# Optimization experiments

Measured on AMD Instinct MI355X. Metric: run time of the kernel, lower is better.

## Reference

```python
import jax, jax.numpy as jnp
import numpy as np

B, S, D, H = 2, 2048, 1024, 16
DH = D // H  # 64
NEG = -1000000000.0


def setup_inputs() -> dict:
    key = jax.random.key(0)
    ks = jax.random.split(key, 10)
    scale = 1.0 / np.sqrt(D)
    inp = {
        "x": jax.random.normal(ks[0], (B, S, D), dtype=jnp.float32),
        "mask": jax.random.randint(ks[1], (B, S, S), 0, 2, dtype=jnp.int32),
        "Wq": jax.random.normal(ks[2], (D, D), dtype=jnp.float32) * scale,
        "bq": jnp.zeros((D,), dtype=jnp.float32),
        "Wk": jax.random.normal(ks[3], (D, D), dtype=jnp.float32) * scale,
        "bk": jnp.zeros((D,), dtype=jnp.float32),
        "Wv": jax.random.normal(ks[4], (D, D), dtype=jnp.float32) * scale,
        "bv": jnp.zeros((D,), dtype=jnp.float32),
        "Wo": jax.random.normal(ks[5], (D, D), dtype=jnp.float32) * scale,
        "bo": jnp.zeros((D,), dtype=jnp.float32),
    }
    return inp


def reference(x, mask, Wq, bq, Wk, bk, Wv, bv, Wo, bo):
    b, s, _ = x.shape
    # Linear projections (torch Linear: y = x @ W^T + b), then split heads -> [b,h,s,dh]
    q = (x @ Wq.T + bq).reshape(b, s, H, DH).transpose(0, 2, 1, 3)
    k = (x @ Wk.T + bk).reshape(b, s, H, DH).transpose(0, 2, 1, 3)
    v = (x @ Wv.T + bv).reshape(b, s, H, DH).transpose(0, 2, 1, 3)
    # scores: [b,h,sq,sk]
    scores = jnp.einsum("bhqd,bhkd->bhqk", q, k) / jnp.sqrt(jnp.float32(DH))
    # code masks where mask == 0 (mask broadcast over heads)
    scores = jnp.where(mask[:, None, :, :] == 0, NEG, scores)
    attn = jax.nn.softmax(scores, axis=-1)
    out = jnp.einsum("bhqk,bhkd->bhqd", attn, v)  # [b,h,sq,dh]
    out = out.transpose(0, 2, 1, 3).reshape(b, s, D)  # merge heads -> [b,s,d]
    return out @ Wo.T + bo
```

## Files before the change

### kernel.cpp

```cpp
#include <hip/hip_runtime.h>
#include <stdint.h>

#define SB 2
#define SS 2048
#define SD 1024
#define SH 16
#define SDH 64
#define SM (SB*SS)
#define NEGINF_MASK -1000000000.0f
#define QSCALE 0.18033688011112043f
#define CSHIFT 16.0f

typedef __attribute__((ext_vector_type(8))) short short8;
typedef __attribute__((ext_vector_type(4))) short short4v;
typedef __attribute__((ext_vector_type(4))) float f32x4;
typedef __attribute__((ext_vector_type(4))) float float4v;
typedef __attribute__((ext_vector_type(4))) uint32_t uint4v;

__device__ static inline short f2bf(float f) {
    uint32_t u = __float_as_uint(f);
    u += 0x7fffu + ((u >> 16) & 1u);
    return (short)(u >> 16);
}

__device__ static inline void gload_lds16(const void* g, void* l) {
    __builtin_amdgcn_global_load_lds(
        (__attribute__((address_space(1))) void*)g,
        (__attribute__((address_space(3))) void*)l,
        16, 0, 0);
}

#define NX4 (SM*SD/4)
#define NW4 (SD*SD/4)
__global__ void cvt_all_kernel(const float* __restrict__ x,
                               const float* __restrict__ Wq, const float* __restrict__ Wk,
                               const float* __restrict__ Wv, const float* __restrict__ Wo,
                               short* __restrict__ xb,
                               short* __restrict__ wqb, short* __restrict__ wkb,
                               short* __restrict__ wvb, short* __restrict__ wob) {
    int i = blockIdx.x * 256 + threadIdx.x;
    const float* src; short* dst; int idx;
    if (i < NX4) { src = x; dst = xb; idx = i; }
    else {
        int j = i - NX4;
        int sel = j >> 18;
        idx = j & (NW4 - 1);
        src = (sel == 0) ? Wq : (sel == 1) ? Wk : (sel == 2) ? Wv : Wo;
        dst = (sel == 0) ? wqb : (sel == 1) ? wkb : (sel == 2) ? wvb : wob;
    }
    float4v v = *(const float4v*)(src + (size_t)idx * 4);
    short4v o;
    o[0] = f2bf(v[0]); o[1] = f2bf(v[1]); o[2] = f2bf(v[2]); o[3] = f2bf(v[3]);
    *(short4v*)(dst + (size_t)idx * 4) = o;
}

__global__ void pack_mask_kernel(const int* __restrict__ mask, unsigned long long* __restrict__ bits) {
    unsigned int i = blockIdx.x * 256u + threadIdx.x;
    int pred = mask[i] != 0;
    unsigned long long b = __ballot(pred);
    if ((threadIdx.x & 63u) == 0u) bits[i >> 6] = b;
}

__global__ __launch_bounds__(256, 3) void gemm_qkv_kernel(
    const short* __restrict__ A,
    const short* __restrict__ W0, const short* __restrict__ W1, const short* __restrict__ W2,
    const float* __restrict__ b0, const float* __restrict__ b1, const float* __restrict__ b2,
    short* __restrict__ O0, short* __restrict__ O1, short* __restrict__ O2) {
    const short* W = (blockIdx.z == 0) ? W0 : (blockIdx.z == 1) ? W1 : W2;
    const float* bias = (blockIdx.z == 0) ? b0 : (blockIdx.z == 1) ? b1 : b2;
    short* C = (blockIdx.z == 0) ? O0 : (blockIdx.z == 1) ? O1 : O2;
    const float scale = (blockIdx.z == 0) ? QSCALE : 1.0f;
    const int rowBase = blockIdx.y * 128, colBase = blockIdx.x * 128;
    const int K = SD, N = SD;

    __shared__ short As[2][128 * 32];
    __shared__ short Bs[2][128 * 32];
    const int tid = threadIdx.x, lane = tid & 63, wid = tid >> 6;
    const int r15 = lane & 15, hi = lane >> 4;
    const int wr = wid >> 1, wc = wid & 1;

    const int chBase0 = wid * 64, chBase1 = 256 + wid * 64;
    const int ch0 = chBase0 + lane, ch1 = chBase1 + lane;
    const short* aP0 = A + (size_t)(rowBase + (ch0 >> 2)) * K + (ch0 & 3) * 8;
    const short* aP1 = A + (size_t)(rowBase + (ch1 >> 2)) * K + (ch1 & 3) * 8;
    const short* bP0 = W + (size_t)(colBase + (ch0 >> 2)) * K + (ch0 & 3) * 8;
    const short* bP1 = W + (size_t)(colBase + (ch1 >> 2)) * K + (ch1 & 3) * 8;

    gload_lds16(aP0, &As[0][chBase0 * 8]);
    gload_lds16(aP1, &As[0][chBase1 * 8]);
    gload_lds16(bP0, &Bs[0][chBase0 * 8]);
    gload_lds16(bP1, &Bs[0][chBase1 * 8]);

    f32x4 acc[4][4] = {};
    const int NIT = K / 32;

    for (int it = 0; it < NIT; ++it) {
        __syncthreads();
        const int cur = it & 1, nxt = cur ^ 1;
        if (it + 1 < NIT) {
            int kt = (it + 1) * 32;
            gload_lds16(aP0 + kt, &As[nxt][chBase0 * 8]);
            gload_lds16(aP1 + kt, &As[nxt][chBase1 * 8]);
            gload_lds16(bP0 + kt, &Bs[nxt][chBase0 * 8]);
            gload_lds16(bP1 + kt, &Bs[nxt][chBase1 * 8]);
        }

        short8 aF[4], bF[4];
#pragma unroll
        for (int mi = 0; mi < 4; ++mi)
            aF[mi] = *(const short8*)&As[cur][(wr * 64 + mi * 16 + r15) * 32 + hi * 8];
#pragma unroll
        for (int ni = 0; ni < 4; ++ni)
            bF[ni] = *(const short8*)&Bs[cur][(wc * 64 + ni * 16 + r15) * 32 + hi * 8];

        __builtin_amdgcn_s_setprio(1);
#pragma unroll
        for (int mi = 0; mi < 4; ++mi)
#pragma unroll
            for (int ni = 0; ni < 4; ++ni)
                acc[mi][ni] = __builtin_amdgcn_mfma_f32_16x16x32_bf16(aF[mi], bF[ni], acc[mi][ni], 0, 0, 0);
        __builtin_amdgcn_s_setprio(0);
    }

#pragma unroll
    for (int ni = 0; ni < 4; ++ni) {
        int col = colBase + wc * 64 + ni * 16 + r15;
        float bv = bias[col];
#pragma unroll
        for (int mi = 0; mi < 4; ++mi) {
#pragma unroll
            for (int r = 0; r < 4; ++r) {
                int row = rowBase + wr * 64 + mi * 16 + hi * 4 + r;
                C[(size_t)row * N + col] = f2bf((acc[mi][ni][r] + bv) * scale);
            }
        }
    }
}

__global__ __launch_bounds__(256, 2) void gemm_out_kernel(
    const short* __restrict__ A, const short* __restrict__ W,
    const float* __restrict__ bias, float* __restrict__ C) {
    const int rowBase = blockIdx.y * 128, colBase = blockIdx.x * 64;
    const int K = SD, N = SD;

    __shared__ short As[2][128 * 32];
    __shared__ short Bs[2][64 * 32];
    const int tid = threadIdx.x, lane = tid & 63, wid = tid >> 6;
    const int r15 = lane & 15, hi = lane >> 4;

    const int chBase0 = wid * 64, chBase1 = 256 + wid * 64;
    const int ch0 = chBase0 + lane, ch1 = chBase1 + lane;
    const short* aP0 = A + (size_t)(rowBase + (ch0 >> 2)) * K + (ch0 & 3) * 8;
    const short* aP1 = A + (size_t)(rowBase + (ch1 >> 2)) * K + (ch1 & 3) * 8;
    const short* bP0 = W + (size_t)(colBase + (ch0 >> 2)) * K + (ch0 & 3) * 8;

    gload_lds16(aP0, &As[0][chBase0 * 8]);
    gload_lds16(aP1, &As[0][chBase1 * 8]);
    gload_lds16(bP0, &Bs[0][chBase0 * 8]);

    f32x4 acc[2][4] = {};
    const int NIT = K / 32;

    for (int it = 0; it < NIT; ++it) {
        __syncthreads();
        const int cur = it & 1, nxt = cur ^ 1;
        if (it + 1 < NIT) {
            int kt = (it + 1) * 32;
            gload_lds16(aP0 + kt, &As[nxt][chBase0 * 8]);
            gload_lds16(aP1 + kt, &As[nxt][chBase1 * 8]);
            gload_lds16(bP0 + kt, &Bs[nxt][chBase0 * 8]);
        }

        short8 aF[2], bF[4];
#pragma unroll
        for (int mi = 0; mi < 2; ++mi)
            aF[mi] = *(const short8*)&As[cur][(wid * 32 + mi * 16 + r15) * 32 + hi * 8];
#pragma unroll
        for (int ni = 0; ni < 4; ++ni)
            bF[ni] = *(const short8*)&Bs[cur][(ni * 16 + r15) * 32 + hi * 8];

        __builtin_amdgcn_s_setprio(1);
#pragma unroll
        for (int mi = 0; mi < 2; ++mi)
#pragma unroll
            for (int ni = 0; ni < 4; ++ni)
                acc[mi][ni] = __builtin_amdgcn_mfma_f32_16x16x32_bf16(aF[mi], bF[ni], acc[mi][ni], 0, 0, 0);
        __builtin_amdgcn_s_setprio(0);
    }

#pragma unroll
    for (int ni = 0; ni < 4; ++ni) {
        int col = colBase + ni * 16 + r15;
        float bv = bias[col];
#pragma unroll
        for (int mi = 0; mi < 2; ++mi) {
#pragma unroll
            for (int r = 0; r < 4; ++r) {
                int row = rowBase + wid * 32 + mi * 16 + hi * 4 + r;
                C[(size_t)row * N + col] = acc[mi][ni][r] + bv;
            }
        }
    }
}

__global__ __launch_bounds__(512, 4) void attn_kernel(
    const short* __restrict__ Q, const short* __restrict__ K, const short* __restrict__ V,
    const unsigned long long* __restrict__ mbits, short* __restrict__ O) {
    const int tid = threadIdx.x, lane = tid & 63, wid = tid >> 6;
    const int r15 = lane & 15, hi = lane >> 4;
    const int b = blockIdx.z, h = blockIdx.y;
    const int q0 = blockIdx.x * 128 + wid * 16;
    const int brow = b * SS;

    __shared__ short Ks[2][64 * 64];
    __shared__ short Vt[2][64 * 72];

    const short* Kbase = K + (size_t)brow * SD + h * SDH;
    const short* Vbase = V + (size_t)brow * SD + h * SDH;
    const unsigned long long* mrow_p = mbits + (size_t)(brow + q0 + r15) * (SS / 64);

    short8 qF[2];
#pragma unroll
    for (int kd = 0; kd < 2; ++kd)
        qF[kd] = *(const short8*)&Q[(size_t)(brow + q0 + r15) * SD + h * SDH + kd * 32 + hi * 8];

    short8 onesF;
#pragma unroll
    for (int j = 0; j < 8; ++j) onesF[j] = (short)0x3F80;

    f32x4 o[4] = {};
    f32x4 lacc = {};

    const int krow_s = tid >> 3, kcol_s = tid & 7;
    const int vp = tid & 31, vc0 = (tid >> 5) * 4;
    const int k2 = 2 * vp;
    const int vcol = (k2 & 32) | ((k2 & 12) << 1) | ((k2 & 16) >> 2) | (k2 & 3);

    gload_lds16(Kbase + (size_t)krow_s * SD + ((kcol_s ^ (krow_s & 7)) * 8), &Ks[0][wid * 512]);
    short4v va = *(const short4v*)(Vbase + (size_t)k2 * SD + vc0);
    short4v vb2 = *(const short4v*)(Vbase + (size_t)(k2 + 1) * SD + vc0);
    unsigned long long mb = mrow_p[0];
#pragma unroll
    for (int j = 0; j < 4; ++j) {
        uint32_t pk = (uint32_t)(uint16_t)va[j] | ((uint32_t)(uint16_t)vb2[j] << 16);
        *(uint32_t*)&Vt[0][(vc0 + j) * 72 + vcol] = pk;
    }

    for (int t = 0; t < SS / 64; ++t) {
        __syncthreads();
        const int cur = t & 1, nxt = cur ^ 1;
        const int tn = (t < SS / 64 - 1) ? t + 1 : t;

        gload_lds16(Kbase + (size_t)(tn * 64 + krow_s) * SD + ((kcol_s ^ (krow_s & 7)) * 8),
                    &Ks[nxt][wid * 512]);
        va  = *(const short4v*)(Vbase + (size_t)(tn * 64 + k2) * SD + vc0);
        vb2 = *(const short4v*)(Vbase + (size_t)(tn * 64 + k2 + 1) * SD + vc0);
        unsigned long long mbn = mrow_p[tn];

        f32x4 s[4] = {};
        __builtin_amdgcn_s_setprio(1);
#pragma unroll
        for (int kc = 0; kc < 4; ++kc) {
            int krow = kc * 16 + r15;
#pragma unroll
            for (int kd = 0; kd < 2; ++kd) {
                short8 kF = *(const short8*)&Ks[cur][krow * 64 + (((kd * 4 + hi) ^ (krow & 7)) * 8)];
                s[kc] = __builtin_amdgcn_mfma_f32_16x16x32_bf16(kF, qF[kd], s[kc], 0, 0, 0);
            }
        }
        __builtin_amdgcn_s_setprio(0);

#pragma unroll
        for (int kc = 0; kc < 4; ++kc) {
            unsigned nib = (unsigned)(mb >> (kc * 16 + hi * 4)) & 0xFu;
#pragma unroll
            for (int r = 0; r < 4; ++r) {
                float v = (nib & (1u << r)) ? (s[kc][r] - CSHIFT) : NEGINF_MASK;
                float e;
                asm("v_exp_f32 %0, %1" : "=v"(e) : "v"(v));
                s[kc][r] = e;
            }
        }

        short8 pF[2];
#pragma unroll
        for (int kf = 0; kf < 2; ++kf) {
            uint32_t w0, w1, w2, w3;
            asm("v_cvt_pk_bf16_f32 %0, %1, %2" : "=v"(w0) : "v"(s[2 * kf][0]),     "v"(s[2 * kf][1]));
            asm("v_cvt_pk_bf16_f32 %0, %1, %2" : "=v"(w1) : "v"(s[2 * kf][2]),     "v"(s[2 * kf][3]));
            asm("v_cvt_pk_bf16_f32 %0, %1, %2" : "=v"(w2) : "v"(s[2 * kf + 1][0]), "v"(s[2 * kf + 1][1]));
            asm("v_cvt_pk_bf16_f32 %0, %1, %2" : "=v"(w3) : "v"(s[2 * kf + 1][2]), "v"(s[2 * kf + 1][3]));
            uint4v t4 = { w0, w1, w2, w3 };
            pF[kf] = __builtin_bit_cast(short8, t4);
        }

        __builtin_amdgcn_s_setprio(1);
#pragma unroll
        for (int df = 0; df < 4; ++df) {
#pragma unroll
            for (int kf = 0; kf < 2; ++kf) {
                short8 vF = *(const short8*)&Vt[cur][(df * 16 + r15) * 72 + kf * 32 + hi * 8];
                o[df] = __builtin_amdgcn_mfma_f32_16x16x32_bf16(pF[kf], vF, o[df], 0, 0, 0);
            }
        }
        lacc = __builtin_amdgcn_mfma_f32_16x16x32_bf16(pF[0], onesF, lacc, 0, 0, 0);
        lacc = __builtin_amdgcn_mfma_f32_16x16x32_bf16(pF[1], onesF, lacc, 0, 0, 0);
        __builtin_amdgcn_s_setprio(0);

#pragma unroll
        for (int j = 0; j < 4; ++j) {
            uint32_t pk = (uint32_t)(uint16_t)va[j] | ((uint32_t)(uint16_t)vb2[j] << 16);
            *(uint32_t*)&Vt[nxt][(vc0 + j) * 72 + vcol] = pk;
        }
        mb = mbn;
    }

#pragma unroll
    for (int r = 0; r < 4; ++r) {
        float inv = 1.0f / lacc[r];
        size_t row = (size_t)(brow + q0 + hi * 4 + r);
#pragma unroll
        for (int df = 0; df < 4; ++df)
            O[row * SD + h * SDH + df * 16 + r15] = f2bf(o[df][r] * inv);
    }
}

extern "C" void kernel_launch(void* const* d_in, const int* in_sizes, int n_in,
                              void* d_out, int out_size, void* d_ws, size_t ws_size,
                              hipStream_t stream) {
    const float* x  = (const float*)d_in[0];
    const int* mask = (const int*)d_in[1];
    const float* Wq = (const float*)d_in[2];
    const float* bq = (const float*)d_in[3];
    const float* Wk = (const float*)d_in[4];
    const float* bk = (const float*)d_in[5];
    const float* Wv = (const float*)d_in[6];
    const float* bv = (const float*)d_in[7];
    const float* Wo = (const float*)d_in[8];
    const float* bo = (const float*)d_in[9];
    float* out = (float*)d_out;

    char* ws = (char*)d_ws;
    size_t off = 0;
    auto alloc = [&](size_t bytes) { void* p = ws + off; off += (bytes + 255) & ~(size_t)255; return p; };

    short* xb  = (short*)alloc((size_t)SM * SD * 2);
    short* wqb = (short*)alloc((size_t)SD * SD * 2);
    short* wkb = (short*)alloc((size_t)SD * SD * 2);
    short* wvb = (short*)alloc((size_t)SD * SD * 2);
    short* wob = (short*)alloc((size_t)SD * SD * 2);
    short* Qb  = (short*)alloc((size_t)SM * SD * 2);
    short* Kb  = (short*)alloc((size_t)SM * SD * 2);
    short* Vb  = (short*)alloc((size_t)SM * SD * 2);
    short* AOb = (short*)alloc((size_t)SM * SD * 2);
    unsigned long long* mbits = (unsigned long long*)alloc((size_t)SB * SS * (SS / 64) * 8);

    cvt_all_kernel<<<(NX4 + 4 * NW4) / 256, 256, 0, stream>>>(
        x, Wq, Wk, Wv, Wo, xb, wqb, wkb, wvb, wob);
    pack_mask_kernel<<<SB * SS * SS / 256, 256, 0, stream>>>(mask, mbits);

    gemm_qkv_kernel<<<dim3(SD / 128, SM / 128, 3), 256, 0, stream>>>(
        xb, wqb, wkb, wvb, bq, bk, bv, Qb, Kb, Vb);

    attn_kernel<<<dim3(SS / 128, SH, SB), 512, 0, stream>>>(Qb, Kb, Vb, mbits, AOb);

    gemm_out_kernel<<<dim3(SD / 64, SM / 128), 256, 0, stream>>>(AOb, wob, bo, out);
}
```

Measured before the change: 142.8 us.

## Swizzle block order for XCD locality, fuse prep kernels, cheapen mask-exp

Remaps block indices in the QKV GEMM, output GEMM and attention kernels so that neighbouring tiles land on the same XCD, improving L2 reuse of shared operands. Merges the bf16 conversion and mask bit-packing into a single launch to save launch overhead. In attention, computes exp unconditionally and zeros masked entries with a bitwise AND, and drops the constant shift before the exp. Dropping the shift relies on scores staying in range and on normalisation absorbing the removed constant.

```diff
diff --git a/kernel.cpp b/kernel.cpp
--- a/kernel.cpp
+++ b/kernel.cpp
@@ -7,9 +7,7 @@
 #define SH 16
 #define SDH 64
 #define SM (SB*SS)
-#define NEGINF_MASK -1000000000.0f
 #define QSCALE 0.18033688011112043f
-#define CSHIFT 16.0f
 
 typedef __attribute__((ext_vector_type(8))) short short8;
 typedef __attribute__((ext_vector_type(4))) short short4v;
@@ -32,33 +30,37 @@
 
 #define NX4 (SM*SD/4)
 #define NW4 (SD*SD/4)
-__global__ void cvt_all_kernel(const float* __restrict__ x,
-                               const float* __restrict__ Wq, const float* __restrict__ Wk,
-                               const float* __restrict__ Wv, const float* __restrict__ Wo,
-                               short* __restrict__ xb,
-                               short* __restrict__ wqb, short* __restrict__ wkb,
-                               short* __restrict__ wvb, short* __restrict__ wob) {
-    int i = blockIdx.x * 256 + threadIdx.x;
-    const float* src; short* dst; int idx;
-    if (i < NX4) { src = x; dst = xb; idx = i; }
-    else {
-        int j = i - NX4;
-        int sel = j >> 18;
-        idx = j & (NW4 - 1);
-        src = (sel == 0) ? Wq : (sel == 1) ? Wk : (sel == 2) ? Wv : Wo;
-        dst = (sel == 0) ? wqb : (sel == 1) ? wkb : (sel == 2) ? wvb : wob;
-    }
-    float4v v = *(const float4v*)(src + (size_t)idx * 4);
-    short4v o;
-    o[0] = f2bf(v[0]); o[1] = f2bf(v[1]); o[2] = f2bf(v[2]); o[3] = f2bf(v[3]);
-    *(short4v*)(dst + (size_t)idx * 4) = o;
-}
-
-__global__ void pack_mask_kernel(const int* __restrict__ mask, unsigned long long* __restrict__ bits) {
-    unsigned int i = blockIdx.x * 256u + threadIdx.x;
-    int pred = mask[i] != 0;
-    unsigned long long b = __ballot(pred);
-    if ((threadIdx.x & 63u) == 0u) bits[i >> 6] = b;
+#define NCVT (NX4 + 4*NW4)
+#define NMSK (SB*SS*SS)
+__global__ void prep_kernel(const float* __restrict__ x,
+                            const float* __restrict__ Wq, const float* __restrict__ Wk,
+                            const float* __restrict__ Wv, const float* __restrict__ Wo,
+                            const int* __restrict__ mask,
+                            short* __restrict__ xb,
+                            short* __restrict__ wqb, short* __restrict__ wkb,
+                            short* __restrict__ wvb, short* __restrict__ wob,
+                            unsigned long long* __restrict__ bits) {
+    unsigned i = blockIdx.x * 256u + threadIdx.x;
+    if (i < NCVT) {
+        const float* src; short* dst; unsigned idx;
+        if (i < NX4) { src = x; dst = xb; idx = i; }
+        else {
+            unsigned j = i - NX4;
+            unsigned sel = j >> 18;
+            idx = j & (NW4 - 1);
+            src = (sel == 0) ? Wq : (sel == 1) ? Wk : (sel == 2) ? Wv : Wo;
+            dst = (sel == 0) ? wqb : (sel == 1) ? wkb : (sel == 2) ? wvb : wob;
+        }
+        float4v v = *(const float4v*)(src + (size_t)idx * 4);
+        short4v o;
+        o[0] = f2bf(v[0]); o[1] = f2bf(v[1]); o[2] = f2bf(v[2]); o[3] = f2bf(v[3]);
+        *(short4v*)(dst + (size_t)idx * 4) = o;
+    } else {
+        unsigned j = i - NCVT;
+        int pred = mask[j] != 0;
+        unsigned long long bb = __ballot(pred);
+        if ((threadIdx.x & 63u) == 0u) bits[j >> 6] = bb;
+    }
 }
 
 __global__ __launch_bounds__(256, 3) void gemm_qkv_kernel(
@@ -66,11 +68,15 @@
     const short* __restrict__ W0, const short* __restrict__ W1, const short* __restrict__ W2,
     const float* __restrict__ b0, const float* __restrict__ b1, const float* __restrict__ b2,
     short* __restrict__ O0, short* __restrict__ O1, short* __restrict__ O2) {
-    const short* W = (blockIdx.z == 0) ? W0 : (blockIdx.z == 1) ? W1 : W2;
-    const float* bias = (blockIdx.z == 0) ? b0 : (blockIdx.z == 1) ? b1 : b2;
-    short* C = (blockIdx.z == 0) ? O0 : (blockIdx.z == 1) ? O1 : O2;
-    const float scale = (blockIdx.z == 0) ? QSCALE : 1.0f;
-    const int rowBase = blockIdx.y * 128, colBase = blockIdx.x * 128;
+    unsigned flat = blockIdx.x + (blockIdx.y << 3) + (blockIdx.z << 8);
+    unsigned swz = (flat & 7u) * 96u + (flat >> 3);
+    const int bx = swz & 7, by = (swz >> 3) & 31, bz = swz >> 8;
+
+    const short* W = (bz == 0) ? W0 : (bz == 1) ? W1 : W2;
+    const float* bias = (bz == 0) ? b0 : (bz == 1) ? b1 : b2;
+    short* C = (bz == 0) ? O0 : (bz == 1) ? O1 : O2;
+    const float scale = (bz == 0) ? QSCALE : 1.0f;
+    const int rowBase = by * 128, colBase = bx * 128;
     const int K = SD, N = SD;
 
     __shared__ short As[2][128 * 32];
@@ -140,7 +146,9 @@
 __global__ __launch_bounds__(256, 2) void gemm_out_kernel(
     const short* __restrict__ A, const short* __restrict__ W,
     const float* __restrict__ bias, float* __restrict__ C) {
-    const int rowBase = blockIdx.y * 128, colBase = blockIdx.x * 64;
+    unsigned flat = blockIdx.x + (blockIdx.y << 4);
+    unsigned swz = (flat & 7u) * 64u + (flat >> 3);
+    const int rowBase = ((swz >> 4) & 31) * 128, colBase = (swz & 15) * 64;
     const int K = SD, N = SD;
 
     __shared__ short As[2][128 * 32];
@@ -206,10 +214,13 @@
 __global__ __launch_bounds__(512, 4) void attn_kernel(
     const short* __restrict__ Q, const short* __restrict__ K, const short* __restrict__ V,
     const unsigned long long* __restrict__ mbits, short* __restrict__ O) {
+    unsigned flat = blockIdx.x + (blockIdx.y << 4) + (blockIdx.z << 8);
+    unsigned swz = (flat & 7u) * 64u + (flat >> 3);
+    const int bx = swz & 15, h = (swz >> 4) & 15, b = swz >> 8;
+
     const int tid = threadIdx.x, lane = tid & 63, wid = tid >> 6;
     const int r15 = lane & 15, hi = lane >> 4;
-    const int b = blockIdx.z, h = blockIdx.y;
-    const int q0 = blockIdx.x * 128 + wid * 16;
+    const int q0 = bx * 128 + wid * 16;
     const int brow = b * SS;
 
     __shared__ short Ks[2][64 * 64];
@@ -235,6 +246,7 @@
     const int vp = tid & 31, vc0 = (tid >> 5) * 4;
     const int k2 = 2 * vp;
     const int vcol = (k2 & 32) | ((k2 & 12) << 1) | ((k2 & 16) >> 2) | (k2 & 3);
+    const int sh4 = hi * 4;
 
     gload_lds16(Kbase + (size_t)krow_s * SD + ((kcol_s ^ (krow_s & 7)) * 8), &Ks[0][wid * 512]);
     short4v va = *(const short4v*)(Vbase + (size_t)k2 * SD + vc0);
@@ -270,15 +282,20 @@
         }
         __builtin_amdgcn_s_setprio(0);
 
-#pragma unroll
-        for (int kc = 0; kc < 4; ++kc) {
-            unsigned nib = (unsigned)(mb >> (kc * 16 + hi * 4)) & 0xFu;
-#pragma unroll
-            for (int r = 0; r < 4; ++r) {
-                float v = (nib & (1u << r)) ? (s[kc][r] - CSHIFT) : NEGINF_MASK;
-                float e;
-                asm("v_exp_f32 %0, %1" : "=v"(e) : "v"(v));
-                s[kc][r] = e;
+        {
+            unsigned lo32 = (unsigned)mb, hi32 = (unsigned)(mb >> 32);
+            unsigned hsh[4] = { lo32 >> sh4, (lo32 >> 16) >> sh4,
+                                hi32 >> sh4, (hi32 >> 16) >> sh4 };
+#pragma unroll
+            for (int kc = 0; kc < 4; ++kc) {
+                unsigned hh = hsh[kc];
+#pragma unroll
+                for (int r = 0; r < 4; ++r) {
+                    float e;
+                    asm("v_exp_f32 %0, %1" : "=v"(e) : "v"(s[kc][r]));
+                    int m = ((int)(hh << (31 - r))) >> 31;
+                    s[kc][r] = __uint_as_float(__float_as_uint(e) & (unsigned)m);
+                }
             }
         }
 
@@ -355,9 +372,8 @@
     short* AOb = (short*)alloc((size_t)SM * SD * 2);
     unsigned long long* mbits = (unsigned long long*)alloc((size_t)SB * SS * (SS / 64) * 8);
 
-    cvt_all_kernel<<<(NX4 + 4 * NW4) / 256, 256, 0, stream>>>(
-        x, Wq, Wk, Wv, Wo, xb, wqb, wkb, wvb, wob);
-    pack_mask_kernel<<<SB * SS * SS / 256, 256, 0, stream>>>(mask, mbits);
+    prep_kernel<<<(NCVT + NMSK) / 256, 256, 0, stream>>>(
+        x, Wq, Wk, Wv, Wo, mask, xb, wqb, wkb, wvb, wob, mbits);
 
     gemm_qkv_kernel<<<dim3(SD / 128, SM / 128, 3), 256, 0, stream>>>(
         xb, wqb, wkb, wvb, bq, bk, bv, Qb, Kb, Vb);
```

Result: faster. 135.7 us (-5.0%).
